# Optimization experiments

Hardware: AMD Instinct MI355X
Metric: run time of the kernel (lower is better)

The kernel has to match this reference:

```python
import jax, jax.numpy as jnp
import numpy as np
from jax import lax

BN_EPS = 1e-5
PAD = ((2, 3), (1, 2))  # 'same' padding for kernel (6,4): H pad 5 -> (2,3), W pad 3 -> (1,2)
DN = ('NCHW', 'OIHW', 'NCHW')


def _conv_block(x, w, b, g, bt, m, v, pool):
    # pool(bn(relu(conv(pad(x))))) as in the torch module (eval-mode BN)
    x = lax.conv_general_dilated(x, w, (1, 1), PAD, dimension_numbers=DN)
    x = jax.nn.relu(x + b[None, :, None, None])
    scale = g / jnp.sqrt(v + BN_EPS)
    x = (x - m[None, :, None, None]) * scale[None, :, None, None] + bt[None, :, None, None]
    win = (1, 1) + pool
    return lax.reduce_window(x, -jnp.inf, lax.max, win, win, 'VALID')


def _fc_bn(x, w, b, g, bt, m, v):
    x = jax.nn.relu(x @ w.T + b)
    return (x - m) * (g / jnp.sqrt(v + BN_EPS)) + bt


def _apply_cnn(x, p):
    x = x[:, None, :, :]  # [N,1,72,64]
    x = _conv_block(x, p['conv1_w'], p['conv1_b'], p['bnc1_g'], p['bnc1_b'], p['bnc1_m'], p['bnc1_v'], (2, 2))
    x = _conv_block(x, p['conv2_w'], p['conv2_b'], p['bnc2_g'], p['bnc2_b'], p['bnc2_m'], p['bnc2_v'], (2, 2))
    x = _conv_block(x, p['conv3_w'], p['conv3_b'], p['bnc3_g'], p['bnc3_b'], p['bnc3_m'], p['bnc3_v'], (3, 4))
    x = x.reshape(x.shape[0], 6 * 4 * 64)  # NCHW contiguous flatten matches torch .view
    x = _fc_bn(x, p['fc1_w'], p['fc1_b'], p['bnf1_g'], p['bnf1_b'], p['bnf1_m'], p['bnf1_v'])
    x = _fc_bn(x, p['fc2_w'], p['fc2_b'], p['bnf2_g'], p['bnf2_b'], p['bnf2_m'], p['bnf2_v'])
    x = _fc_bn(x, p['fc3_w'], p['fc3_b'], p['bnf3_g'], p['bnf3_b'], p['bnf3_m'], p['bnf3_v'])
    # F.normalize(x, p=2, dim=1) with eps=1e-12
    nrm = jnp.linalg.norm(x, axis=1, keepdims=True)
    return x / jnp.maximum(nrm, 1e-12)


def _ssm(embeds):
    # pairwise L2 distances via Gram trick (replaces the O(n^2) python loop)
    sq = jnp.sum(embeds * embeds, axis=1)  # [n]
    d2 = sq[:, None] + sq[None, :] - 2.0 * (embeds @ embeds.T)
    dist = jnp.sqrt(jnp.maximum(d2, 1e-12))
    dist = jnp.where(d2 > 0, dist, 0.0)  # exact zeros on diagonal, nan-safe grad
    return dist / jnp.max(dist)


def setup_inputs() -> dict:
    key = jax.random.key(0)
    ks = iter(jax.random.split(key, 64))
    d = {'x': jax.random.normal(next(ks), (512, 72, 64), jnp.float32)}

    def nrm(shape, s=0.05):
        return jax.random.normal(next(ks), shape, jnp.float32) * s

    def add_bn(name, c):
        d[name + '_g'] = 1.0 + nrm((c,))
        d[name + '_b'] = nrm((c,))
        d[name + '_m'] = nrm((c,), 0.1)
        d[name + '_v'] = 0.5 + jax.random.uniform(next(ks), (c,), jnp.float32)

    d['conv1_w'] = nrm((16, 1, 6, 4), 0.2);  d['conv1_b'] = nrm((16,));  add_bn('bnc1', 16)
    d['conv2_w'] = nrm((32, 16, 6, 4), 0.1); d['conv2_b'] = nrm((32,));  add_bn('bnc2', 32)
    d['conv3_w'] = nrm((64, 32, 6, 4), 0.05); d['conv3_b'] = nrm((64,)); add_bn('bnc3', 64)
    d['fc1_w'] = nrm((512, 1536), 0.03); d['fc1_b'] = nrm((512,)); add_bn('bnf1', 512)
    d['fc2_w'] = nrm((256, 512), 0.05);  d['fc2_b'] = nrm((256,)); add_bn('bnf2', 256)
    d['fc3_w'] = nrm((128, 256), 0.07);  d['fc3_b'] = nrm((128,)); add_bn('bnf3', 128)
    return d


def reference(x,
              conv1_w, conv1_b, bnc1_g, bnc1_b, bnc1_m, bnc1_v,
              conv2_w, conv2_b, bnc2_g, bnc2_b, bnc2_m, bnc2_v,
              conv3_w, conv3_b, bnc3_g, bnc3_b, bnc3_m, bnc3_v,
              fc1_w, fc1_b, bnf1_g, bnf1_b, bnf1_m, bnf1_v,
              fc2_w, fc2_b, bnf2_g, bnf2_b, bnf2_m, bnf2_v,
              fc3_w, fc3_b, bnf3_g, bnf3_b, bnf3_m, bnf3_v):
    p = dict(conv1_w=conv1_w, conv1_b=conv1_b, bnc1_g=bnc1_g, bnc1_b=bnc1_b, bnc1_m=bnc1_m, bnc1_v=bnc1_v,
             conv2_w=conv2_w, conv2_b=conv2_b, bnc2_g=bnc2_g, bnc2_b=bnc2_b, bnc2_m=bnc2_m, bnc2_v=bnc2_v,
             conv3_w=conv3_w, conv3_b=conv3_b, bnc3_g=bnc3_g, bnc3_b=bnc3_b, bnc3_m=bnc3_m, bnc3_v=bnc3_v,
             fc1_w=fc1_w, fc1_b=fc1_b, bnf1_g=bnf1_g, bnf1_b=bnf1_b, bnf1_m=bnf1_m, bnf1_v=bnf1_v,
             fc2_w=fc2_w, fc2_b=fc2_b, bnf2_g=bnf2_g, bnf2_b=bnf2_b, bnf2_m=bnf2_m, bnf2_v=bnf2_v,
             fc3_w=fc3_w, fc3_b=fc3_b, bnf3_g=bnf3_g, bnf3_b=bnf3_b, bnf3_m=bnf3_m, bnf3_v=bnf3_v)
    embeds = _apply_cnn(x, p)  # [n, 128], L2-normalized
    return _ssm(embeds)        # [n, n]
```

## Files before the change

kernel.cpp:

```cpp
#include <hip/hip_runtime.h>
#include <math.h>


#define BN_EPS 1e-5f

typedef __attribute__((ext_vector_type(8))) short short8;
typedef __attribute__((ext_vector_type(4))) float f32x4;

__device__ __forceinline__ unsigned short f2bf(float f) {
    unsigned u = __float_as_uint(f);
    u += 0x7fffu + ((u >> 16) & 1u);
    return (unsigned short)(u >> 16);
}

__device__ __forceinline__ short8 f2bf8(float4 lo, float4 hi) {
    short8 r;
    r[0] = (short)f2bf(lo.x); r[1] = (short)f2bf(lo.y);
    r[2] = (short)f2bf(lo.z); r[3] = (short)f2bf(lo.w);
    r[4] = (short)f2bf(hi.x); r[5] = (short)f2bf(hi.y);
    r[6] = (short)f2bf(hi.z); r[7] = (short)f2bf(hi.w);
    return r;
}

__global__ __launch_bounds__(256) void repack_k(
    const float* __restrict__ w1, const float* __restrict__ w2,
    const float* __restrict__ w3,
    const float* __restrict__ fw1, const float* __restrict__ fw2,
    const float* __restrict__ fw3,
    unsigned short* __restrict__ wT1b,
    unsigned short* __restrict__ wT2b, unsigned short* __restrict__ wT3b,
    unsigned short* __restrict__ fw1b, unsigned short* __restrict__ fw2b,
    unsigned short* __restrict__ fw3b, unsigned* __restrict__ mxslot)
{
    int t = blockIdx.x * 256 + threadIdx.x;
    if (t == 0) *mxslot = 0u;
    if (t < 512) {
        int k = t & 31, oc = t >> 5;
        wT1b[t] = (k < 24) ? f2bf(w1[oc * 24 + k]) : (unsigned short)0;
    }
    if (t < 12288) {
        int k = t & 31, oc = (t >> 5) & 31, kk = t >> 10;
        int ky = kk >> 1, kxp = kk & 1;
        int hi = k >> 4, ic = k & 15;
        int kx = 2 * kxp + hi;
        wT2b[t] = f2bf(w2[((oc * 16 + ic) * 6 + ky) * 4 + kx]);
    }
    if (t < 49152) {
        int ic = t & 31, oc = (t >> 5) & 63, kk = t >> 11;
        int ky = kk >> 2, kx = kk & 3;
        wT3b[t] = f2bf(w3[((oc * 32 + ic) * 6 + ky) * 4 + kx]);
    }
    int base = t * 8;
    if (base < 950272) {
        const float* src; unsigned short* dst; int off;
        if (base < 786432)      { src = fw1; dst = fw1b; off = base; }
        else if (base < 917504) { src = fw2; dst = fw2b; off = base - 786432; }
        else                    { src = fw3; dst = fw3b; off = base - 917504; }
        float4 lo = *(const float4*)(src + off);
        float4 hi = *(const float4*)(src + off + 4);
        *(short8*)(dst + off) = f2bf8(lo, hi);
    }
}

__global__ __launch_bounds__(512) void conv_all(
    const float* __restrict__ x, const unsigned short* __restrict__ wT1,
    const unsigned short* __restrict__ wT2, const unsigned short* __restrict__ wT3,
    const float* __restrict__ c1b, const float* __restrict__ g1,
    const float* __restrict__ b1, const float* __restrict__ m1,
    const float* __restrict__ v1,
    const float* __restrict__ c2b, const float* __restrict__ g2,
    const float* __restrict__ b2, const float* __restrict__ m2,
    const float* __restrict__ v2,
    const float* __restrict__ c3b, const float* __restrict__ g3,
    const float* __restrict__ b3, const float* __restrict__ m3,
    const float* __restrict__ v3,
    unsigned short* __restrict__ out3)
{
    __shared__ __align__(16) unsigned short s_out1[2 * 1476 * 8];
    __shared__ __align__(16) unsigned short s_un[4 * 480 * 8];
    const int tid = threadIdx.x, nl = blockIdx.x;
    const int lane = tid & 63, wave = tid >> 6;
    const int n = lane & 15, q = lane >> 4;
    unsigned short* pa = s_un;
    unsigned short* pb = s_un + 5534;

    {
        unsigned* z32 = (unsigned*)s_un;
        for (int i = tid; i < 5532; i += 512) z32[i] = 0u;
        uint4 z4; z4.x = z4.y = z4.z = z4.w = 0u;
        for (int pc = tid; pc < 324; pc += 512) {
            int row, colc;
            if (pc < 180) { row = pc / 36; colc = pc % 36; if (row >= 2) row += 36; }
            else { int pz = pc - 180; row = 2 + (pz >> 2); colc = (pz & 3) ? 32 + (pz & 3) : 0; }
            int cc = row * 36 + colc;
            *(uint4*)(s_out1 + cc * 8) = z4;
            *(uint4*)(s_out1 + 11808 + cc * 8) = z4;
        }
    }
    __syncthreads();
    {
        const float4* src = (const float4*)(x + (size_t)nl * 4608);
        for (int i = tid; i < 1152; i += 512) {
            float4 val = src[i];
            int f = i * 4, row = (f >> 6) + 2, c = (f & 63) + 1;
            unsigned short h0 = f2bf(val.x), h1 = f2bf(val.y);
            unsigned short h2 = f2bf(val.z), h3 = f2bf(val.w);
            unsigned short* ap = pa + row * 70 + c;
            ap[0] = h0; ap[1] = h1; ap[2] = h2; ap[3] = h3;
            unsigned* bp = (unsigned*)(pb + row * 70 + c + 1);
            bp[0] = (unsigned)h0 | ((unsigned)h1 << 16);
            bp[1] = (unsigned)h2 | ((unsigned)h3 << 16);
        }
    }
    const float sc1 = g1[n] * rsqrtf(v1[n] + BN_EPS);
    const float bb1 = c1b[n];
    const float mm1 = b1[n] - m1[n] * sc1;
    const short8 bfr1 = *(const short8*)(wT1 + n * 32 + q * 8);
    __syncthreads();

    for (int i = 0; i < 36; ++i) {
        int t = wave * 36 + i;
        int pooled = 4 * t + (n >> 2);
        int ph = pooled >> 5, pw = pooled & 31;
        int py = (n >> 1) & 1, px = n & 1;
        int oh = 2 * ph + py, ow = 2 * pw + px;
        int r0 = (oh + 2 * q) * 70;
        const unsigned* base = px ? (const unsigned*)(pb + r0 + ow + 1)
                                  : (const unsigned*)(pa + r0 + ow);
        uint4 uu;
        uu.x = base[0];  uu.y = base[1];
        uu.z = base[35]; uu.w = base[36];
        short8 afr = *reinterpret_cast<short8*>(&uu);
        f32x4 acc = (f32x4){0.f, 0.f, 0.f, 0.f};
        acc = __builtin_amdgcn_mfma_f32_16x16x32_bf16(afr, bfr1, acc, 0, 0, 0);
        int po = 4 * t + q, oph = po >> 5, opw = po & 31;
        float mx = fmaxf(fmaxf(acc[0], acc[1]), fmaxf(acc[2], acc[3]));
        float val = fmaxf(mx + bb1, 0.f) * sc1 + mm1;
        int cc = (oph + 2) * 36 + (opw + 1);
        s_out1[(n >> 3) * 11808 + cc * 8 + (n & 7)] = f2bf(val);
    }
    __syncthreads();
    {
        uint4 z4; z4.x = z4.y = z4.z = z4.w = 0u;
        for (int pc = tid; pc < 192; pc += 512) {
            int row, colc;
            if (pc < 120) { row = pc / 20; colc = pc % 20; if (row >= 2) row += 18; }
            else { int pz = pc - 120; row = 2 + (pz >> 2); colc = (pz & 3) ? 16 + (pz & 3) : 0; }
            int cc = row * 20 + colc;
            *(uint4*)(s_un + cc * 8) = z4;
            *(uint4*)(s_un + 3840 + cc * 8) = z4;
            *(uint4*)(s_un + 7680 + cc * 8) = z4;
            *(uint4*)(s_un + 11520 + cc * 8) = z4;
        }
    }
    float bnb2[2], bns2[2], bnm2[2];
#pragma unroll
    for (int nt = 0; nt < 2; ++nt) {
        int oc = nt * 16 + n;
        float sc = g2[oc] * rsqrtf(v2[oc] + BN_EPS);
        bnb2[nt] = c2b[oc]; bns2[nt] = sc; bnm2[nt] = b2[oc] - m2[oc] * sc;
    }
    __syncthreads();

    for (int pp = wave; pp < 36; pp += 8) {
        int ph = pp >> 1, half = pp & 1;
        const unsigned short* bB = s_out1 + (q & 1) * 11808 + (q >> 1) * 8
                                   + (half * 16 + n) * 8 + (2 * ph) * 288;
        f32x4 acc[2][2];
#pragma unroll
        for (int ab = 0; ab < 2; ++ab)
#pragma unroll
            for (int nt = 0; nt < 2; ++nt) acc[ab][nt] = (f32x4){0.f, 0.f, 0.f, 0.f};
#pragma unroll
        for (int ky = 0; ky < 6; ++ky)
#pragma unroll
            for (int kxp = 0; kxp < 2; ++kxp) {
                int kk = ky * 2 + kxp;
                short8 w0 = *(const short8*)(wT2 + ((size_t)(kk * 32 + n) * 32) + q * 8);
                short8 w1 = *(const short8*)(wT2 + ((size_t)(kk * 32 + 16 + n) * 32) + q * 8);
#pragma unroll
                for (int ab = 0; ab < 2; ++ab) {
                    short8 afr = *(const short8*)(bB + ((ab + ky) * 288 + kxp * 16));
                    acc[ab][0] = __builtin_amdgcn_mfma_f32_16x16x32_bf16(afr, w0, acc[ab][0], 0, 0, 0);
                    acc[ab][1] = __builtin_amdgcn_mfma_f32_16x16x32_bf16(afr, w1, acc[ab][1], 0, 0, 0);
                }
            }
        int pw0 = half * 8 + q * 2;
#pragma unroll
        for (int nt = 0; nt < 2; ++nt) {
            int oc = nt * 16 + n;
            float p0 = fmaxf(fmaxf(acc[0][nt][0], acc[0][nt][1]),
                             fmaxf(acc[1][nt][0], acc[1][nt][1]));
            float p1 = fmaxf(fmaxf(acc[0][nt][2], acc[0][nt][3]),
                             fmaxf(acc[1][nt][2], acc[1][nt][3]));
            p0 = fmaxf(p0 + bnb2[nt], 0.f) * bns2[nt] + bnm2[nt];
            p1 = fmaxf(p1 + bnb2[nt], 0.f) * bns2[nt] + bnm2[nt];
            int cellA = (ph + 2) * 20 + pw0 + 1;
            int pl = (oc >> 3) * 3840, cl = oc & 7;
            s_un[pl + cellA * 8 + cl] = f2bf(p0);
            s_un[pl + (cellA + 1) * 8 + cl] = f2bf(p1);
        }
    }
    __syncthreads();

    for (int ch = wave; ch < 12; ch += 8) {
        int pr = ch >> 1, nth = ch & 1;
        const unsigned short* bC = s_un + q * 3840 + n * 8 + (3 * pr) * 160;
        f32x4 acc[3][2];
#pragma unroll
        for (int r = 0; r < 3; ++r)
#pragma unroll
            for (int t2 = 0; t2 < 2; ++t2) acc[r][t2] = (f32x4){0.f, 0.f, 0.f, 0.f};
#pragma unroll
        for (int ky = 0; ky < 6; ++ky)
#pragma unroll
            for (int kx = 0; kx < 4; ++kx) {
                int kk = ky * 4 + kx;
                short8 w0 = *(const short8*)(wT3 + ((size_t)(kk * 64 + nth * 32 + n) * 32) + q * 8);
                short8 w1 = *(const short8*)(wT3 + ((size_t)(kk * 64 + nth * 32 + 16 + n) * 32) + q * 8);
#pragma unroll
                for (int r = 0; r < 3; ++r) {
                    short8 afr = *(const short8*)(bC + ((r + ky) * 160 + kx * 8));
                    acc[r][0] = __builtin_amdgcn_mfma_f32_16x16x32_bf16(afr, w0, acc[r][0], 0, 0, 0);
                    acc[r][1] = __builtin_amdgcn_mfma_f32_16x16x32_bf16(afr, w1, acc[r][1], 0, 0, 0);
                }
            }
        size_t ob = (size_t)nl * 1536;
#pragma unroll
        for (int t2 = 0; t2 < 2; ++t2) {
            int oc = nth * 32 + t2 * 16 + n;
            float sc = g3[oc] * rsqrtf(v3[oc] + BN_EPS);
            float mx = -3.4e38f;
#pragma unroll
            for (int r = 0; r < 3; ++r)
#pragma unroll
                for (int e = 0; e < 4; ++e) mx = fmaxf(mx, acc[r][t2][e]);
            float val = fmaxf(mx + c3b[oc], 0.f) * sc + (b3[oc] - m3[oc] * sc);
            out3[ob + (size_t)oc * 24 + pr * 4 + q] = f2bf(val);
        }
    }
}

__global__ __launch_bounds__(256) void fc_ks(
    const unsigned short* __restrict__ A, const unsigned short* __restrict__ W,
    const float* __restrict__ bias, const float* __restrict__ g,
    const float* __restrict__ bt, const float* __restrict__ m,
    const float* __restrict__ v, unsigned short* __restrict__ out_b,
    float* __restrict__ out_f, int K, int N, int mode)
{
    __shared__ f32x4 part[256];
    const int tid = threadIdx.x;
    const int lane = tid & 63, wave = tid >> 6;
    const int n = lane & 15, q = lane >> 4;
    const int r0 = blockIdx.y * 16;
    const int c0 = blockIdx.x * 16;
    const int col = c0 + n;

    const int Kc = K >> 2;
    const int base = wave * Kc;
    const unsigned short* Ap = A + (size_t)(r0 + n) * K + base + q * 8;
    const unsigned short* Bp = W + (size_t)col * K + base + q * 8;

    f32x4 acc0 = (f32x4){0.f, 0.f, 0.f, 0.f};
    f32x4 acc1 = (f32x4){0.f, 0.f, 0.f, 0.f};
#pragma unroll 2
    for (int kk = 0; kk < Kc; kk += 64) {
        short8 a0 = *(const short8*)(Ap + kk);
        short8 b0 = *(const short8*)(Bp + kk);
        short8 a1 = *(const short8*)(Ap + kk + 32);
        short8 b1 = *(const short8*)(Bp + kk + 32);
        acc0 = __builtin_amdgcn_mfma_f32_16x16x32_bf16(a0, b0, acc0, 0, 0, 0);
        acc1 = __builtin_amdgcn_mfma_f32_16x16x32_bf16(a1, b1, acc1, 0, 0, 0);
    }
    part[tid] = acc0 + acc1;
    __syncthreads();
    if (wave == 0) {
        f32x4 s = part[lane] + part[64 + lane] + part[128 + lane] + part[192 + lane];
        float sc = g[col] * rsqrtf(v[col] + BN_EPS);
        float bb = bias[col];
        float mm = bt[col] - m[col] * sc;
#pragma unroll
        for (int e = 0; e < 4; ++e) {
            int row = r0 + q * 4 + e;
            float val = fmaxf(s[e] + bb, 0.f) * sc + mm;
            if (mode == 0) out_b[(size_t)row * N + col] = f2bf(val);
            else           out_f[(size_t)row * N + col] = val;
        }
    }
}

__global__ __launch_bounds__(128) void norm_k(const float* __restrict__ f3,
                                              float* __restrict__ E,
                                              float* __restrict__ sq)
{
    __shared__ float red[2];
    const int row = blockIdx.x, tid = threadIdx.x;
    float vv = f3[row * 128 + tid];
    float s = vv * vv;
#pragma unroll
    for (int off = 32; off >= 1; off >>= 1) s += __shfl_down(s, off, 64);
    if ((tid & 63) == 0) red[tid >> 6] = s;
    __syncthreads();
    float total = red[0] + red[1];
    float nn = fmaxf(sqrtf(total), 1e-12f);
    E[row * 128 + tid] = vv / nn;
    if (tid == 0) sq[row] = total / (nn * nn);
}

__global__ __launch_bounds__(256) void dist_k(const float* __restrict__ E,
                                              const float* __restrict__ sq,
                                              float* __restrict__ D,
                                              unsigned* __restrict__ mxslot)
{
    __shared__ __align__(16) float Ei[16 * 132];
    __shared__ __align__(16) float Ej[16 * 132];
    __shared__ float red[256];
    const int tid = threadIdx.x;
    const int bi = blockIdx.y * 16, bj = blockIdx.x * 16;
    {
        int lr = tid >> 4, lc = (tid & 15) * 8;
        float4 a0 = *(const float4*)(E + (bi + lr) * 128 + lc);
        float4 a1 = *(const float4*)(E + (bi + lr) * 128 + lc + 4);
        *(float4*)(Ei + lr * 132 + lc) = a0;
        *(float4*)(Ei + lr * 132 + lc + 4) = a1;
        float4 b0 = *(const float4*)(E + (bj + lr) * 128 + lc);
        float4 b1 = *(const float4*)(E + (bj + lr) * 128 + lc + 4);
        *(float4*)(Ej + lr * 132 + lc) = b0;
        *(float4*)(Ej + lr * 132 + lc + 4) = b1;
    }
    __syncthreads();
    const int tx = tid & 15, ty = tid >> 4;
    float dot = 0.f;
#pragma unroll 4
    for (int k = 0; k < 128; k += 4) {
        float4 a = *(const float4*)(Ei + ty * 132 + k);
        float4 b = *(const float4*)(Ej + tx * 132 + k);
        dot = fmaf(a.x, b.x, dot); dot = fmaf(a.y, b.y, dot);
        dot = fmaf(a.z, b.z, dot); dot = fmaf(a.w, b.w, dot);
    }
    int i = bi + ty, j = bj + tx;
    float d2 = sq[i] + sq[j] - 2.f * dot;
    float dist = sqrtf(fmaxf(d2, 1e-12f));
    dist = (d2 > 0.f) ? dist : 0.f;
    if (i == j) dist = 0.f;
    D[i * 512 + j] = dist;
    red[tid] = dist;
    __syncthreads();
    for (int s2 = 128; s2 > 0; s2 >>= 1) {
        if (tid < s2) red[tid] = fmaxf(red[tid], red[tid + s2]);
        __syncthreads();
    }
    if (tid == 0) atomicMax(mxslot, __float_as_uint(red[0]));
}

__global__ __launch_bounds__(256) void scale_k(float* __restrict__ D,
                                               const unsigned* __restrict__ mxslot)
{
    int idx = (blockIdx.x * 256 + threadIdx.x) * 4;
    float M = __uint_as_float(*mxslot);
    float4 d = *(float4*)(D + idx);
    d.x /= M; d.y /= M; d.z /= M; d.w /= M;
    *(float4*)(D + idx) = d;
}

extern "C" void kernel_launch(void* const* d_in, const int* in_sizes, int n_in,
                              void* d_out, int out_size, void* d_ws, size_t ws_size,
                              hipStream_t stream)
{
    (void)in_sizes; (void)n_in; (void)out_size; (void)ws_size;
    const float* x    = (const float*)d_in[0];
    const float* c1w  = (const float*)d_in[1];
    const float* c1b  = (const float*)d_in[2];
    const float* g1   = (const float*)d_in[3];
    const float* b1   = (const float*)d_in[4];
    const float* m1   = (const float*)d_in[5];
    const float* v1   = (const float*)d_in[6];
    const float* c2w  = (const float*)d_in[7];
    const float* c2b  = (const float*)d_in[8];
    const float* g2   = (const float*)d_in[9];
    const float* b2   = (const float*)d_in[10];
    const float* m2   = (const float*)d_in[11];
    const float* v2   = (const float*)d_in[12];
    const float* c3w  = (const float*)d_in[13];
    const float* c3b  = (const float*)d_in[14];
    const float* g3   = (const float*)d_in[15];
    const float* b3   = (const float*)d_in[16];
    const float* m3   = (const float*)d_in[17];
    const float* v3   = (const float*)d_in[18];
    const float* fw1  = (const float*)d_in[19];
    const float* fb1  = (const float*)d_in[20];
    const float* gf1  = (const float*)d_in[21];
    const float* bf1  = (const float*)d_in[22];
    const float* mf1  = (const float*)d_in[23];
    const float* vf1  = (const float*)d_in[24];
    const float* fw2  = (const float*)d_in[25];
    const float* fb2  = (const float*)d_in[26];
    const float* gf2  = (const float*)d_in[27];
    const float* bf2  = (const float*)d_in[28];
    const float* mf2  = (const float*)d_in[29];
    const float* vf2  = (const float*)d_in[30];
    const float* fw3  = (const float*)d_in[31];
    const float* fb3  = (const float*)d_in[32];
    const float* gf3  = (const float*)d_in[33];
    const float* bf3  = (const float*)d_in[34];
    const float* mf3  = (const float*)d_in[35];
    const float* vf3  = (const float*)d_in[36];

    float* ws = (float*)d_ws;
    float* E    = ws + 0;
    float* sq   = ws + 65536;
    float* f3v  = ws + 66048;
    unsigned* mx = (unsigned*)(ws + 131584);
    unsigned short* wT1b = (unsigned short*)(ws + 131600);
    unsigned short* wT2b = (unsigned short*)(ws + 131856);
    unsigned short* wT3b = (unsigned short*)(ws + 138000);
    unsigned short* fw1b = (unsigned short*)(ws + 162576);
    unsigned short* fw2b = (unsigned short*)(ws + 555792);
    unsigned short* fw3b = (unsigned short*)(ws + 621328);
    unsigned short* out3b= (unsigned short*)(ws + 637712);
    unsigned short* a1b  = (unsigned short*)(ws + 1030928);
    unsigned short* a2b  = (unsigned short*)(ws + 1162000);

    float* out = (float*)d_out;

    repack_k<<<464, 256, 0, stream>>>(c1w, c2w, c3w, fw1, fw2, fw3,
                                      wT1b, wT2b, wT3b, fw1b, fw2b, fw3b, mx);
    conv_all<<<512, 512, 0, stream>>>(x, wT1b, wT2b, wT3b,
                                      c1b, g1, b1, m1, v1,
                                      c2b, g2, b2, m2, v2,
                                      c3b, g3, b3, m3, v3, out3b);
    fc_ks<<<dim3(32, 32), 256, 0, stream>>>(out3b, fw1b, fb1, gf1, bf1, mf1, vf1,
                                            a1b, nullptr, 1536, 512, 0);
    fc_ks<<<dim3(16, 32), 256, 0, stream>>>(a1b, fw2b, fb2, gf2, bf2, mf2, vf2,
                                            a2b, nullptr, 512, 256, 0);
    fc_ks<<<dim3(8, 32), 256, 0, stream>>>(a2b, fw3b, fb3, gf3, bf3, mf3, vf3,
                                           nullptr, f3v, 256, 128, 1);
    norm_k<<<512, 128, 0, stream>>>(f3v, E, sq);
    dist_k<<<dim3(32, 32), 256, 0, stream>>>(E, sq, out, mx);
    scale_k<<<256, 256, 0, stream>>>(out, mx);
}
```

Measured before the change: 211.9 us.

## Fuse three FC+BN layers and L2 normalize into one kernel

Replaces three fc_ks launches and norm_k with a single fc_fused kernel. Each block handles 16 rows and keeps the intermediate activations in shared memory across all three layers. This removes three launches and the global round trips for a1/a2/f3. In exchange only 32 blocks run, so parallelism drops sharply and every block streams the full FC weight matrices from global or L2.

```diff
diff --git a/kernel.cpp b/kernel.cpp
--- a/kernel.cpp
+++ b/kernel.cpp
@@ -241,70 +241,153 @@
     }
 }
 
-__global__ __launch_bounds__(256) void fc_ks(
-    const unsigned short* __restrict__ A, const unsigned short* __restrict__ W,
-    const float* __restrict__ bias, const float* __restrict__ g,
-    const float* __restrict__ bt, const float* __restrict__ m,
-    const float* __restrict__ v, unsigned short* __restrict__ out_b,
-    float* __restrict__ out_f, int K, int N, int mode)
+__global__ __launch_bounds__(512) void fc_fused(
+    const unsigned short* __restrict__ A,
+    const unsigned short* __restrict__ W1, const float* __restrict__ fb1,
+    const float* __restrict__ gf1, const float* __restrict__ bf1,
+    const float* __restrict__ mf1, const float* __restrict__ vf1,
+    const unsigned short* __restrict__ W2, const float* __restrict__ fb2,
+    const float* __restrict__ gf2, const float* __restrict__ bf2,
+    const float* __restrict__ mf2, const float* __restrict__ vf2,
+    const unsigned short* __restrict__ W3, const float* __restrict__ fb3,
+    const float* __restrict__ gf3, const float* __restrict__ bf3,
+    const float* __restrict__ mf3, const float* __restrict__ vf3,
+    float* __restrict__ E, float* __restrict__ sq)
 {
-    __shared__ f32x4 part[256];
+    __shared__ __align__(16) unsigned short sA[24576];
+    __shared__ __align__(16) unsigned short sB1[8192];
+    __shared__ __align__(16) unsigned short sB2[4096];
+    __shared__ float sF[16 * 132];
     const int tid = threadIdx.x;
     const int lane = tid & 63, wave = tid >> 6;
     const int n = lane & 15, q = lane >> 4;
-    const int r0 = blockIdx.y * 16;
-    const int c0 = blockIdx.x * 16;
-    const int col = c0 + n;
-
-    const int Kc = K >> 2;
-    const int base = wave * Kc;
-    const unsigned short* Ap = A + (size_t)(r0 + n) * K + base + q * 8;
-    const unsigned short* Bp = W + (size_t)col * K + base + q * 8;
-
-    f32x4 acc0 = (f32x4){0.f, 0.f, 0.f, 0.f};
-    f32x4 acc1 = (f32x4){0.f, 0.f, 0.f, 0.f};
+    const int r0 = blockIdx.x * 16;
+
+    for (int i = tid; i < 3072; i += 512) {
+        int row = i & 15, k8 = i >> 4;
+        *(uint4*)(sA + ((k8 * 16 + row) * 8)) =
+            *(const uint4*)(A + (size_t)(r0 + row) * 1536 + k8 * 8);
+    }
+    __syncthreads();
+
+    {
+        const unsigned short* ap = sA + n * 8 + q * 128;
+        f32x4 acc0[4], acc1[4];
+        const unsigned short* bp[4];
+#pragma unroll
+        for (int j = 0; j < 4; ++j) {
+            acc0[j] = (f32x4){0.f, 0.f, 0.f, 0.f};
+            acc1[j] = (f32x4){0.f, 0.f, 0.f, 0.f};
+            bp[j] = W1 + (size_t)((wave * 4 + j) * 16 + n) * 1536 + q * 8;
+        }
 #pragma unroll 2
-    for (int kk = 0; kk < Kc; kk += 64) {
-        short8 a0 = *(const short8*)(Ap + kk);
-        short8 b0 = *(const short8*)(Bp + kk);
-        short8 a1 = *(const short8*)(Ap + kk + 32);
-        short8 b1 = *(const short8*)(Bp + kk + 32);
-        acc0 = __builtin_amdgcn_mfma_f32_16x16x32_bf16(a0, b0, acc0, 0, 0, 0);
-        acc1 = __builtin_amdgcn_mfma_f32_16x16x32_bf16(a1, b1, acc1, 0, 0, 0);
-    }
-    part[tid] = acc0 + acc1;
-    __syncthreads();
-    if (wave == 0) {
-        f32x4 s = part[lane] + part[64 + lane] + part[128 + lane] + part[192 + lane];
-        float sc = g[col] * rsqrtf(v[col] + BN_EPS);
-        float bb = bias[col];
-        float mm = bt[col] - m[col] * sc;
+        for (int kk = 0; kk < 1536; kk += 64) {
+            short8 a0 = *(const short8*)(ap + kk * 16);
+            short8 a1 = *(const short8*)(ap + kk * 16 + 512);
+#pragma unroll
+            for (int j = 0; j < 4; ++j) {
+                short8 w0 = *(const short8*)(bp[j] + kk);
+                short8 w1 = *(const short8*)(bp[j] + kk + 32);
+                acc0[j] = __builtin_amdgcn_mfma_f32_16x16x32_bf16(a0, w0, acc0[j], 0, 0, 0);
+                acc1[j] = __builtin_amdgcn_mfma_f32_16x16x32_bf16(a1, w1, acc1[j], 0, 0, 0);
+            }
+        }
+#pragma unroll
+        for (int j = 0; j < 4; ++j) {
+            int col = (wave * 4 + j) * 16 + n;
+            float sc = gf1[col] * rsqrtf(vf1[col] + BN_EPS);
+            float bb = fb1[col];
+            float mm = bf1[col] - mf1[col] * sc;
+#pragma unroll
+            for (int e = 0; e < 4; ++e) {
+                int row = q * 4 + e;
+                float val = fmaxf(acc0[j][e] + acc1[j][e] + bb, 0.f) * sc + mm;
+                sB1[((col >> 3) * 16 + row) * 8 + (col & 7)] = f2bf(val);
+            }
+        }
+    }
+    __syncthreads();
+
+    {
+        const unsigned short* ap = sB1 + n * 8 + q * 128;
+        f32x4 acc0[2], acc1[2];
+        const unsigned short* bp[2];
+#pragma unroll
+        for (int j = 0; j < 2; ++j) {
+            acc0[j] = (f32x4){0.f, 0.f, 0.f, 0.f};
+            acc1[j] = (f32x4){0.f, 0.f, 0.f, 0.f};
+            bp[j] = W2 + (size_t)((wave * 2 + j) * 16 + n) * 512 + q * 8;
+        }
+#pragma unroll 2
+        for (int kk = 0; kk < 512; kk += 64) {
+            short8 a0 = *(const short8*)(ap + kk * 16);
+            short8 a1 = *(const short8*)(ap + kk * 16 + 512);
+#pragma unroll
+            for (int j = 0; j < 2; ++j) {
+                short8 w0 = *(const short8*)(bp[j] + kk);
+                short8 w1 = *(const short8*)(bp[j] + kk + 32);
+                acc0[j] = __builtin_amdgcn_mfma_f32_16x16x32_bf16(a0, w0, acc0[j], 0, 0, 0);
+                acc1[j] = __builtin_amdgcn_mfma_f32_16x16x32_bf16(a1, w1, acc1[j], 0, 0, 0);
+            }
+        }
+#pragma unroll
+        for (int j = 0; j < 2; ++j) {
+            int col = (wave * 2 + j) * 16 + n;
+            float sc = gf2[col] * rsqrtf(vf2[col] + BN_EPS);
+            float bb = fb2[col];
+            float mm = bf2[col] - mf2[col] * sc;
+#pragma unroll
+            for (int e = 0; e < 4; ++e) {
+                int row = q * 4 + e;
+                float val = fmaxf(acc0[j][e] + acc1[j][e] + bb, 0.f) * sc + mm;
+                sB2[((col >> 3) * 16 + row) * 8 + (col & 7)] = f2bf(val);
+            }
+        }
+    }
+    __syncthreads();
+
+    {
+        const unsigned short* ap = sB2 + n * 8 + q * 128;
+        f32x4 acc0 = (f32x4){0.f, 0.f, 0.f, 0.f};
+        f32x4 acc1 = (f32x4){0.f, 0.f, 0.f, 0.f};
+        const unsigned short* bp = W3 + (size_t)(wave * 16 + n) * 256 + q * 8;
+#pragma unroll
+        for (int kk = 0; kk < 256; kk += 64) {
+            short8 a0 = *(const short8*)(ap + kk * 16);
+            short8 a1 = *(const short8*)(ap + kk * 16 + 512);
+            short8 w0 = *(const short8*)(bp + kk);
+            short8 w1 = *(const short8*)(bp + kk + 32);
+            acc0 = __builtin_amdgcn_mfma_f32_16x16x32_bf16(a0, w0, acc0, 0, 0, 0);
+            acc1 = __builtin_amdgcn_mfma_f32_16x16x32_bf16(a1, w1, acc1, 0, 0, 0);
+        }
+        int col = wave * 16 + n;
+        float sc = gf3[col] * rsqrtf(vf3[col] + BN_EPS);
+        float bb = fb3[col];
+        float mm = bf3[col] - mf3[col] * sc;
 #pragma unroll
         for (int e = 0; e < 4; ++e) {
-            int row = r0 + q * 4 + e;
-            float val = fmaxf(s[e] + bb, 0.f) * sc + mm;
-            if (mode == 0) out_b[(size_t)row * N + col] = f2bf(val);
-            else           out_f[(size_t)row * N + col] = val;
-        }
-    }
-}
-
-__global__ __launch_bounds__(128) void norm_k(const float* __restrict__ f3,
-                                              float* __restrict__ E,
-                                              float* __restrict__ sq)
-{
-    __shared__ float red[2];
-    const int row = blockIdx.x, tid = threadIdx.x;
-    float vv = f3[row * 128 + tid];
-    float s = vv * vv;
-#pragma unroll
-    for (int off = 32; off >= 1; off >>= 1) s += __shfl_down(s, off, 64);
-    if ((tid & 63) == 0) red[tid >> 6] = s;
-    __syncthreads();
-    float total = red[0] + red[1];
-    float nn = fmaxf(sqrtf(total), 1e-12f);
-    E[row * 128 + tid] = vv / nn;
-    if (tid == 0) sq[row] = total / (nn * nn);
+            int row = q * 4 + e;
+            sF[row * 132 + col] = fmaxf(acc0[e] + acc1[e] + bb, 0.f) * sc + mm;
+        }
+    }
+    __syncthreads();
+
+    {
+        int row = tid >> 5, g = tid & 31;
+        float v0 = sF[row * 132 + g];
+        float v1 = sF[row * 132 + g + 32];
+        float v2 = sF[row * 132 + g + 64];
+        float v3 = sF[row * 132 + g + 96];
+        float s = v0 * v0 + v1 * v1 + v2 * v2 + v3 * v3;
+#pragma unroll
+        for (int mk = 1; mk <= 16; mk <<= 1) s += __shfl_xor(s, mk, 32);
+        float nn = fmaxf(sqrtf(s), 1e-12f);
+        float inv = 1.f / nn;
+        float* Er = E + (size_t)(r0 + row) * 128;
+        Er[g] = v0 * inv; Er[g + 32] = v1 * inv;
+        Er[g + 64] = v2 * inv; Er[g + 96] = v3 * inv;
+        if (g == 0) sq[r0 + row] = s / (nn * nn);
+    }
 }
 
 __global__ __launch_bounds__(256) void dist_k(const float* __restrict__ E,
@@ -409,7 +492,6 @@
     float* ws = (float*)d_ws;
     float* E    = ws + 0;
     float* sq   = ws + 65536;
-    float* f3v  = ws + 66048;
     unsigned* mx = (unsigned*)(ws + 131584);
     unsigned short* wT1b = (unsigned short*)(ws + 131600);
     unsigned short* wT2b = (unsigned short*)(ws + 131856);
@@ -418,8 +500,6 @@
     unsigned short* fw2b = (unsigned short*)(ws + 555792);
     unsigned short* fw3b = (unsigned short*)(ws + 621328);
     unsigned short* out3b= (unsigned short*)(ws + 637712);
-    unsigned short* a1b  = (unsigned short*)(ws + 1030928);
-    unsigned short* a2b  = (unsigned short*)(ws + 1162000);
 
     float* out = (float*)d_out;
 
@@ -429,13 +509,11 @@
                                       c1b, g1, b1, m1, v1,
                                       c2b, g2, b2, m2, v2,
                                       c3b, g3, b3, m3, v3, out3b);
-    fc_ks<<<dim3(32, 32), 256, 0, stream>>>(out3b, fw1b, fb1, gf1, bf1, mf1, vf1,
-                                            a1b, nullptr, 1536, 512, 0);
-    fc_ks<<<dim3(16, 32), 256, 0, stream>>>(a1b, fw2b, fb2, gf2, bf2, mf2, vf2,
-                                            a2b, nullptr, 512, 256, 0);
-    fc_ks<<<dim3(8, 32), 256, 0, stream>>>(a2b, fw3b, fb3, gf3, bf3, mf3, vf3,
-                                           nullptr, f3v, 256, 128, 1);
-    norm_k<<<512, 128, 0, stream>>>(f3v, E, sq);
+    fc_fused<<<32, 512, 0, stream>>>(out3b,
+                                     fw1b, fb1, gf1, bf1, mf1, vf1,
+                                     fw2b, fb2, gf2, bf2, mf2, vf2,
+                                     fw3b, fb3, gf3, bf3, mf3, vf3,
+                                     E, sq);
     dist_k<<<dim3(32, 32), 256, 0, stream>>>(E, sq, out, mx);
     scale_k<<<256, 256, 0, stream>>>(out, mx);
 }
```

After: 248.1 us. +17.1%, slower.
